# Kernel optimization log

Measured on AMD Instinct MI355X. Metric: run time of the kernel, lower is better.

The kernel has to match this reference:

```python
import jax, jax.numpy as jnp
import numpy as np

NEG_INF = -9e15  # matches torch's -9000000000000000.0 mask value
ALPHA = 0.2      # LeakyReLU negative slope


def setup_inputs() -> dict:
    key = jax.random.key(0)
    k1, k2, k3, k4 = jax.random.split(key, 4)
    B, N, Fin, Fout, H = 32, 512, 256, 64, 8
    x = jax.random.normal(k1, (B, N, Fin), dtype=jnp.float32)
    adj = (jax.random.uniform(k2, (B, N, N)) < 0.5).astype(jnp.float32)
    # W: Linear(in_features, out_features*n_heads, bias=False) weight, stored as (Fin, Fout*H)
    W = jax.random.normal(k3, (Fin, Fout * H), dtype=jnp.float32) / np.sqrt(Fin).astype(np.float32)
    # a: attention vector per head over concat(src,dst) features -> (H, 2*Fout)
    a = jax.random.normal(k4, (H, 2 * Fout), dtype=jnp.float32) * 0.1
    return {"x": x, "adj": adj, "W": W, "a": a}


def reference(x, adj, W, a):
    # x: (B,N,Fin), adj: (B,N,N), W: (Fin, H*F), a: (H, 2F)
    B, N, _ = x.shape
    H, twoF = a.shape
    F = twoF // 2
    h = (x @ W).reshape(B, N, H, F)  # (B,N,H,F)
    # Decompose concat-score: e_ij = lrelu(h_i . a_src + h_j . a_dst) -- same math
    # as (cat(h_i,h_j) * a).sum(-1) without materializing (B,N,N,H,2F).
    s_src = jnp.einsum('bnhf,hf->bnh', h, a[:, :F])  # (B,N,H)
    s_dst = jnp.einsum('bnhf,hf->bnh', h, a[:, F:])  # (B,N,H)
    e = s_src[:, :, None, :] + s_dst[:, None, :, :]  # (B,N,N,H)
    e = jax.nn.leaky_relu(e, negative_slope=ALPHA)
    e = jnp.where(adj[..., None] > 0, e, NEG_INF)
    attn = jax.nn.softmax(e, axis=2)  # softmax over neighbors j (dim=2)
    # dropout omitted (eval mode / p effectively 0 for the reference baseline)
    h_prime = jnp.einsum('bijh,bjhf->bihf', attn, h)  # (B,N,H,F)
    return h_prime.reshape(B, N, H * F)  # concat=True
```

## Files before the change

kernel.cpp:

```cpp
#include <hip/hip_runtime.h>
#include <hip/hip_bf16.h>


#define ALPHA  0.2f
#define ESCALE 1.4426950408889634f

typedef __bf16 bf16x8 __attribute__((ext_vector_type(8)));
typedef __bf16 bf16x4 __attribute__((ext_vector_type(4)));
typedef float  f32x4  __attribute__((ext_vector_type(4)));

#if __has_builtin(__builtin_amdgcn_exp2f)
#define EXP2(x) __builtin_amdgcn_exp2f(x)
#else
#define EXP2(x) exp2f(x)
#endif

#define HT_STRIDE 520
#define WT_STRIDE 264

struct Smem {
    __bf16 hT[64][HT_STRIDE];
    __bf16 WT[64][WT_STRIDE];
    float  ssrc[512], sdst[512];
    float  asrc[64], adst[64];
};

__device__ inline bf16x8 ld8(const float* p) {
    float4 a0 = *(const float4*)p;
    float4 a1 = *(const float4*)(p + 4);
    bf16x8 r;
    r[0]=(__bf16)a0.x; r[1]=(__bf16)a0.y; r[2]=(__bf16)a0.z; r[3]=(__bf16)a0.w;
    r[4]=(__bf16)a1.x; r[5]=(__bf16)a1.y; r[6]=(__bf16)a1.z; r[7]=(__bf16)a1.w;
    return r;
}

__global__ __launch_bounds__(1024, 4) void k_gat(const float* __restrict__ x,
                                                 const float* __restrict__ adj,
                                                 const float* __restrict__ W,
                                                 const float* __restrict__ a,
                                                 float* __restrict__ out) {
    __shared__ Smem sm;
    const int b = blockIdx.x, h = blockIdx.y;
    const int tid  = threadIdx.x;
    const int wave = tid >> 6, lane = tid & 63;
    const int quad = lane >> 4, col = lane & 15;

    if (tid < 128) {
        float v = a[h * 128 + tid] * ESCALE;
        if (tid < 64) sm.asrc[tid] = v; else sm.adst[tid - 64] = v;
    }
    {
        int c = tid & 63, k0 = tid >> 6;
        #pragma unroll 4
        for (int t = 0; t < 16; ++t)
            sm.WT[c][k0 + t * 16] = (__bf16)W[(long)(k0 + t * 16) * 512 + h * 64 + c];
    }
    __syncthreads();

    {
        const float* xb = x + (long)b * 512 * 256;
        f32x4 acc[2][4] = {};
        for (int ks = 0; ks < 8; ++ks) {
            int k0 = ks * 32 + quad * 8;
            bf16x8 av[2], bv[4];
            #pragma unroll
            for (int it = 0; it < 2; ++it)
                av[it] = ld8(xb + (long)(wave * 32 + it * 16 + col) * 256 + k0);
            #pragma unroll
            for (int nt = 0; nt < 4; ++nt)
                bv[nt] = *(const bf16x8*)(&sm.WT[nt * 16 + col][k0]);
            #pragma unroll
            for (int it = 0; it < 2; ++it)
                #pragma unroll
                for (int nt = 0; nt < 4; ++nt)
                    acc[it][nt] = __builtin_amdgcn_mfma_f32_16x16x32_bf16(av[it], bv[nt], acc[it][nt], 0, 0, 0);
        }
        #pragma unroll
        for (int it = 0; it < 2; ++it)
            #pragma unroll
            for (int nt = 0; nt < 4; ++nt) {
                int f = nt * 16 + col;
                int j = wave * 32 + it * 16 + quad * 4;
                bf16x4 pk = { (__bf16)acc[it][nt][0], (__bf16)acc[it][nt][1],
                              (__bf16)acc[it][nt][2], (__bf16)acc[it][nt][3] };
                *(bf16x4*)(&sm.hT[f][j]) = pk;
            }
    }
    __syncthreads();

    {
        int j = tid & 511;
        float s = 0.f;
        if (tid < 512) {
            #pragma unroll 8
            for (int f = 0; f < 64; ++f)
                s += (float)sm.hT[f][j] * sm.asrc[f];
            sm.ssrc[j] = s;
        } else {
            #pragma unroll 8
            for (int f = 0; f < 64; ++f)
                s += (float)sm.hT[f][j] * sm.adst[f];
            sm.sdst[j] = s;
        }
    }
    __syncthreads();

    {
        float si[2];
        const float* arow[2];
        #pragma unroll
        for (int it = 0; it < 2; ++it) {
            int i = wave * 32 + it * 16 + col;
            si[it]   = sm.ssrc[i];
            arow[it] = adj + ((long)b * 512 + i) * 512;
        }
        bf16x8 ones;
        #pragma unroll
        for (int u = 0; u < 8; ++u) ones[u] = (__bf16)1.0f;

        f32x4 acc[2][4] = {};
        f32x4 accs[2]   = {};
        float4 pa0[2], pa1[2];
        #pragma unroll
        for (int it = 0; it < 2; ++it) {
            pa0[it] = *(const float4*)(arow[it] + quad * 8);
            pa1[it] = *(const float4*)(arow[it] + quad * 8 + 4);
        }
        for (int ks = 0; ks < 16; ++ks) {
            int j0 = ks * 32 + quad * 8;
            f32x4 s0 = *(const f32x4*)&sm.sdst[j0];
            f32x4 s1 = *(const f32x4*)&sm.sdst[j0 + 4];
            float sd[8] = {s0[0],s0[1],s0[2],s0[3],s1[0],s1[1],s1[2],s1[3]};
            float am[2][8];
            #pragma unroll
            for (int it = 0; it < 2; ++it) {
                am[it][0]=pa0[it].x; am[it][1]=pa0[it].y;
                am[it][2]=pa0[it].z; am[it][3]=pa0[it].w;
                am[it][4]=pa1[it].x; am[it][5]=pa1[it].y;
                am[it][6]=pa1[it].z; am[it][7]=pa1[it].w;
            }
            if (ks < 15) {
                #pragma unroll
                for (int it = 0; it < 2; ++it) {
                    pa0[it] = *(const float4*)(arow[it] + j0 + 32);
                    pa1[it] = *(const float4*)(arow[it] + j0 + 36);
                }
            }
            bf16x8 P[2];
            #pragma unroll
            for (int it = 0; it < 2; ++it)
                #pragma unroll
                for (int u = 0; u < 8; ++u) {
                    float e = si[it] + sd[u];
                    float l = fmaxf(e, ALPHA * e);
                    float p = am[it][u] * EXP2(l);
                    P[it][u] = (__bf16)p;
                }
            bf16x8 bv[4];
            #pragma unroll
            for (int nt = 0; nt < 4; ++nt)
                bv[nt] = *(const bf16x8*)(&sm.hT[nt * 16 + col][j0]);
            #pragma unroll
            for (int it = 0; it < 2; ++it) {
                #pragma unroll
                for (int nt = 0; nt < 4; ++nt)
                    acc[it][nt] = __builtin_amdgcn_mfma_f32_16x16x32_bf16(P[it], bv[nt], acc[it][nt], 0, 0, 0);
                accs[it] = __builtin_amdgcn_mfma_f32_16x16x32_bf16(P[it], ones, accs[it], 0, 0, 0);
            }
        }
        #pragma unroll
        for (int it = 0; it < 2; ++it)
            #pragma unroll
            for (int r = 0; r < 4; ++r) {
                float s = accs[it][r];
                float inv = (s > 0.f) ? 1.0f / s : 0.f;
                int i = wave * 32 + it * 16 + quad * 4 + r;
                float* orow = out + ((long)b * 512 + i) * 512 + h * 64;
                #pragma unroll
                for (int nt = 0; nt < 4; ++nt)
                    orow[nt * 16 + col] = acc[it][nt][r] * inv;
            }
    }
}

extern "C" void kernel_launch(void* const* d_in, const int* in_sizes, int n_in,
                              void* d_out, int out_size, void* d_ws, size_t ws_size,
                              hipStream_t stream) {
    const float* x   = (const float*)d_in[0];
    const float* adj = (const float*)d_in[1];
    const float* W   = (const float*)d_in[2];
    const float* a   = (const float*)d_in[3];
    float* out = (float*)d_out;
    (void)d_ws; (void)ws_size;

    k_gat<<<dim3(32, 8), 1024, 0, stream>>>(x, adj, W, a, out);
}
```

Measured before the change: 141.2 us.

## Split each (batch, head) block into two 512-thread halves over query rows

Launches twice as many blocks of 512 threads, each handling half of the 512 query rows for a (batch, head) pair. Each block still recomputes the full projected features h and the attention scores, and the hT and WT shared buffers are now a union to cut LDS use. The intent is better occupancy and CU coverage (512 blocks instead of 256). The cost is that the x@W projection is computed twice per pair, and an extra barrier is needed before reusing the union storage.

```diff
diff --git a/kernel.cpp b/kernel.cpp
--- a/kernel.cpp
+++ b/kernel.cpp
@@ -19,8 +19,10 @@
 #define WT_STRIDE 264
 
 struct Smem {
-    __bf16 hT[64][HT_STRIDE];
-    __bf16 WT[64][WT_STRIDE];
+    union {
+        __bf16 hT[64][HT_STRIDE];
+        __bf16 WT[64][WT_STRIDE];
+    } u;
     float  ssrc[512], sdst[512];
     float  asrc[64], adst[64];
 };
@@ -34,13 +36,15 @@
     return r;
 }
 
-__global__ __launch_bounds__(1024, 4) void k_gat(const float* __restrict__ x,
-                                                 const float* __restrict__ adj,
-                                                 const float* __restrict__ W,
-                                                 const float* __restrict__ a,
-                                                 float* __restrict__ out) {
+__global__ __launch_bounds__(512, 4) void k_gat(const float* __restrict__ x,
+                                                const float* __restrict__ adj,
+                                                const float* __restrict__ W,
+                                                const float* __restrict__ a,
+                                                float* __restrict__ out) {
     __shared__ Smem sm;
-    const int b = blockIdx.x, h = blockIdx.y;
+    const int b    = blockIdx.x;
+    const int h    = blockIdx.y >> 1;
+    const int half = blockIdx.y & 1;
     const int tid  = threadIdx.x;
     const int wave = tid >> 6, lane = tid & 63;
     const int quad = lane >> 4, col = lane & 15;
@@ -52,65 +56,65 @@
     {
         int c = tid & 63, k0 = tid >> 6;
         #pragma unroll 4
-        for (int t = 0; t < 16; ++t)
-            sm.WT[c][k0 + t * 16] = (__bf16)W[(long)(k0 + t * 16) * 512 + h * 64 + c];
-    }
-    __syncthreads();
-
+        for (int t = 0; t < 32; ++t)
+            sm.u.WT[c][k0 + t * 8] = (__bf16)W[(long)(k0 + t * 8) * 512 + h * 64 + c];
+    }
+    __syncthreads();
+
+    f32x4 acc1[4][4] = {};
     {
         const float* xb = x + (long)b * 512 * 256;
-        f32x4 acc[2][4] = {};
         for (int ks = 0; ks < 8; ++ks) {
             int k0 = ks * 32 + quad * 8;
-            bf16x8 av[2], bv[4];
-            #pragma unroll
-            for (int it = 0; it < 2; ++it)
-                av[it] = ld8(xb + (long)(wave * 32 + it * 16 + col) * 256 + k0);
+            bf16x8 av[4], bv[4];
+            #pragma unroll
+            for (int it = 0; it < 4; ++it)
+                av[it] = ld8(xb + (long)(wave * 64 + it * 16 + col) * 256 + k0);
             #pragma unroll
             for (int nt = 0; nt < 4; ++nt)
-                bv[nt] = *(const bf16x8*)(&sm.WT[nt * 16 + col][k0]);
-            #pragma unroll
-            for (int it = 0; it < 2; ++it)
+                bv[nt] = *(const bf16x8*)(&sm.u.WT[nt * 16 + col][k0]);
+            #pragma unroll
+            for (int it = 0; it < 4; ++it)
                 #pragma unroll
                 for (int nt = 0; nt < 4; ++nt)
-                    acc[it][nt] = __builtin_amdgcn_mfma_f32_16x16x32_bf16(av[it], bv[nt], acc[it][nt], 0, 0, 0);
-        }
-        #pragma unroll
-        for (int it = 0; it < 2; ++it)
+                    acc1[it][nt] = __builtin_amdgcn_mfma_f32_16x16x32_bf16(av[it], bv[nt], acc1[it][nt], 0, 0, 0);
+        }
+    }
+    __syncthreads();
+    {
+        #pragma unroll
+        for (int it = 0; it < 4; ++it)
             #pragma unroll
             for (int nt = 0; nt < 4; ++nt) {
                 int f = nt * 16 + col;
-                int j = wave * 32 + it * 16 + quad * 4;
-                bf16x4 pk = { (__bf16)acc[it][nt][0], (__bf16)acc[it][nt][1],
-                              (__bf16)acc[it][nt][2], (__bf16)acc[it][nt][3] };
-                *(bf16x4*)(&sm.hT[f][j]) = pk;
-            }
-    }
-    __syncthreads();
-
-    {
-        int j = tid & 511;
-        float s = 0.f;
-        if (tid < 512) {
-            #pragma unroll 8
-            for (int f = 0; f < 64; ++f)
-                s += (float)sm.hT[f][j] * sm.asrc[f];
-            sm.ssrc[j] = s;
-        } else {
-            #pragma unroll 8
-            for (int f = 0; f < 64; ++f)
-                s += (float)sm.hT[f][j] * sm.adst[f];
-            sm.sdst[j] = s;
-        }
-    }
-    __syncthreads();
-
-    {
+                int j = wave * 64 + it * 16 + quad * 4;
+                bf16x4 pk = { (__bf16)acc1[it][nt][0], (__bf16)acc1[it][nt][1],
+                              (__bf16)acc1[it][nt][2], (__bf16)acc1[it][nt][3] };
+                *(bf16x4*)(&sm.u.hT[f][j]) = pk;
+            }
+    }
+    __syncthreads();
+
+    {
+        float as = 0.f, ad = 0.f;
+        #pragma unroll 8
+        for (int f = 0; f < 64; ++f) {
+            float v = (float)sm.u.hT[f][tid];
+            as += v * sm.asrc[f];
+            ad += v * sm.adst[f];
+        }
+        sm.ssrc[tid] = as;
+        sm.sdst[tid] = ad;
+    }
+    __syncthreads();
+
+    {
+        const int row0 = half * 256 + wave * 32;
         float si[2];
         const float* arow[2];
         #pragma unroll
         for (int it = 0; it < 2; ++it) {
-            int i = wave * 32 + it * 16 + col;
+            int i = row0 + it * 16 + col;
             si[it]   = sm.ssrc[i];
             arow[it] = adj + ((long)b * 512 + i) * 512;
         }
@@ -159,7 +163,7 @@
             bf16x8 bv[4];
             #pragma unroll
             for (int nt = 0; nt < 4; ++nt)
-                bv[nt] = *(const bf16x8*)(&sm.hT[nt * 16 + col][j0]);
+                bv[nt] = *(const bf16x8*)(&sm.u.hT[nt * 16 + col][j0]);
             #pragma unroll
             for (int it = 0; it < 2; ++it) {
                 #pragma unroll
@@ -174,7 +178,7 @@
             for (int r = 0; r < 4; ++r) {
                 float s = accs[it][r];
                 float inv = (s > 0.f) ? 1.0f / s : 0.f;
-                int i = wave * 32 + it * 16 + quad * 4 + r;
+                int i = row0 + it * 16 + quad * 4 + r;
                 float* orow = out + ((long)b * 512 + i) * 512 + h * 64;
                 #pragma unroll
                 for (int nt = 0; nt < 4; ++nt)
@@ -193,5 +197,5 @@
     float* out = (float*)d_out;
     (void)d_ws; (void)ws_size;
 
-    k_gat<<<dim3(32, 8), 1024, 0, stream>>>(x, adj, W, a, out);
+    k_gat<<<dim3(32, 16), 512, 0, stream>>>(x, adj, W, a, out);
 }
```

After: 153.6 us. 8.8% more time.

## Split GAT kernel into projection GEMM and row-tiled attention kernels via workspace

Applied to the files above, without the earlier changes.

Splits the fused kernel into two. The first computes the projected features h (bf16, transposed) plus per-node src/dst scores into workspace, computing the scores with shuffles instead of a shared-memory pass. The second launches 4x more, smaller blocks (row quarters) for the masked softmax and aggregation, reading h from global/L2 instead of LDS. This is meant to raise occupancy and parallelism beyond 256 large blocks, at the cost of a global round trip for h and a second launch. The old fused kernel is kept as a fallback when the workspace is too small.

```diff
diff --git a/kernel.cpp b/kernel.cpp
--- a/kernel.cpp
+++ b/kernel.cpp
@@ -17,13 +17,6 @@
 
 #define HT_STRIDE 520
 #define WT_STRIDE 264
-
-struct Smem {
-    __bf16 hT[64][HT_STRIDE];
-    __bf16 WT[64][WT_STRIDE];
-    float  ssrc[512], sdst[512];
-    float  asrc[64], adst[64];
-};
 
 __device__ inline bf16x8 ld8(const float* p) {
     float4 a0 = *(const float4*)p;
@@ -34,12 +27,18 @@
     return r;
 }
 
-__global__ __launch_bounds__(1024, 4) void k_gat(const float* __restrict__ x,
-                                                 const float* __restrict__ adj,
-                                                 const float* __restrict__ W,
-                                                 const float* __restrict__ a,
-                                                 float* __restrict__ out) {
-    __shared__ Smem sm;
+struct SmemK1 {
+    __bf16 WT[64][WT_STRIDE];
+    float  asrc[64], adst[64];
+};
+
+__global__ __launch_bounds__(512, 4) void k1_gemm(const float* __restrict__ x,
+                                                  const float* __restrict__ W,
+                                                  const float* __restrict__ a,
+                                                  __bf16* __restrict__ hT,
+                                                  float* __restrict__ ssrc,
+                                                  float* __restrict__ sdst) {
+    __shared__ SmemK1 sm;
     const int b = blockIdx.x, h = blockIdx.y;
     const int tid  = threadIdx.x;
     const int wave = tid >> 6, lane = tid & 63;
@@ -52,11 +51,200 @@
     {
         int c = tid & 63, k0 = tid >> 6;
         #pragma unroll 4
+        for (int t = 0; t < 32; ++t)
+            sm.WT[c][k0 + t * 8] = (__bf16)W[(long)(k0 + t * 8) * 512 + h * 64 + c];
+    }
+    __syncthreads();
+
+    f32x4 acc[4][4] = {};
+    {
+        const float* xb = x + (long)b * 512 * 256;
+        for (int ks = 0; ks < 8; ++ks) {
+            int k0 = ks * 32 + quad * 8;
+            bf16x8 av[4], bv[4];
+            #pragma unroll
+            for (int it = 0; it < 4; ++it)
+                av[it] = ld8(xb + (long)(wave * 64 + it * 16 + col) * 256 + k0);
+            #pragma unroll
+            for (int nt = 0; nt < 4; ++nt)
+                bv[nt] = *(const bf16x8*)(&sm.WT[nt * 16 + col][k0]);
+            #pragma unroll
+            for (int it = 0; it < 4; ++it)
+                #pragma unroll
+                for (int nt = 0; nt < 4; ++nt)
+                    acc[it][nt] = __builtin_amdgcn_mfma_f32_16x16x32_bf16(av[it], bv[nt], acc[it][nt], 0, 0, 0);
+        }
+    }
+
+    const long bh = (long)b * 8 + h;
+    {
+        #pragma unroll
+        for (int it = 0; it < 4; ++it)
+            #pragma unroll
+            for (int nt = 0; nt < 4; ++nt) {
+                int f = nt * 16 + col;
+                int j = wave * 64 + it * 16 + quad * 4;
+                bf16x4 pk = { (__bf16)acc[it][nt][0], (__bf16)acc[it][nt][1],
+                              (__bf16)acc[it][nt][2], (__bf16)acc[it][nt][3] };
+                *(bf16x4*)(hT + (bh * 64 + f) * 512 + j) = pk;
+            }
+    }
+
+    {
+        float asr[4], adr[4];
+        #pragma unroll
+        for (int nt = 0; nt < 4; ++nt) {
+            asr[nt] = sm.asrc[nt * 16 + col];
+            adr[nt] = sm.adst[nt * 16 + col];
+        }
+        #pragma unroll
+        for (int it = 0; it < 4; ++it)
+            #pragma unroll
+            for (int r = 0; r < 4; ++r) {
+                float ps = 0.f, pd = 0.f;
+                #pragma unroll
+                for (int nt = 0; nt < 4; ++nt) {
+                    ps += acc[it][nt][r] * asr[nt];
+                    pd += acc[it][nt][r] * adr[nt];
+                }
+                #pragma unroll
+                for (int m = 1; m <= 8; m <<= 1) {
+                    ps += __shfl_xor(ps, m, 64);
+                    pd += __shfl_xor(pd, m, 64);
+                }
+                if (col == 0) {
+                    int j = wave * 64 + it * 16 + quad * 4 + r;
+                    ssrc[bh * 512 + j] = ps;
+                    sdst[bh * 512 + j] = pd;
+                }
+            }
+    }
+}
+
+__global__ __launch_bounds__(256, 4) void k2_attn(const float* __restrict__ adj,
+                                                  const __bf16* __restrict__ hT,
+                                                  const float* __restrict__ ssrc,
+                                                  const float* __restrict__ sdst,
+                                                  float* __restrict__ out) {
+    __shared__ float sds[512];
+    const int b = blockIdx.x, h = blockIdx.y, q = blockIdx.z;
+    const int tid  = threadIdx.x;
+    const int wave = tid >> 6, lane = tid & 63;
+    const int quad = lane >> 4, col = lane & 15;
+    const long bh = (long)b * 8 + h;
+    const int rowbase = q * 128 + wave * 32;
+
+    sds[tid]       = sdst[bh * 512 + tid];
+    sds[tid + 256] = sdst[bh * 512 + tid + 256];
+
+    float si[2];
+    const float* arow[2];
+    #pragma unroll
+    for (int it = 0; it < 2; ++it) {
+        int i = rowbase + it * 16 + col;
+        si[it]   = ssrc[bh * 512 + i];
+        arow[it] = adj + ((long)b * 512 + i) * 512;
+    }
+    __syncthreads();
+
+    bf16x8 ones;
+    #pragma unroll
+    for (int u = 0; u < 8; ++u) ones[u] = (__bf16)1.0f;
+
+    f32x4 acc[2][4] = {};
+    f32x4 accs[2]   = {};
+    float4 pa0[2], pa1[2];
+    #pragma unroll
+    for (int it = 0; it < 2; ++it) {
+        pa0[it] = *(const float4*)(arow[it] + quad * 8);
+        pa1[it] = *(const float4*)(arow[it] + quad * 8 + 4);
+    }
+    const __bf16* hTb = hT + bh * 64 * 512;
+    for (int ks = 0; ks < 16; ++ks) {
+        int j0 = ks * 32 + quad * 8;
+        f32x4 s0 = *(const f32x4*)&sds[j0];
+        f32x4 s1 = *(const f32x4*)&sds[j0 + 4];
+        float sd[8] = {s0[0],s0[1],s0[2],s0[3],s1[0],s1[1],s1[2],s1[3]};
+        float am[2][8];
+        #pragma unroll
+        for (int it = 0; it < 2; ++it) {
+            am[it][0]=pa0[it].x; am[it][1]=pa0[it].y;
+            am[it][2]=pa0[it].z; am[it][3]=pa0[it].w;
+            am[it][4]=pa1[it].x; am[it][5]=pa1[it].y;
+            am[it][6]=pa1[it].z; am[it][7]=pa1[it].w;
+        }
+        if (ks < 15) {
+            #pragma unroll
+            for (int it = 0; it < 2; ++it) {
+                pa0[it] = *(const float4*)(arow[it] + j0 + 32);
+                pa1[it] = *(const float4*)(arow[it] + j0 + 36);
+            }
+        }
+        bf16x8 P[2];
+        #pragma unroll
+        for (int it = 0; it < 2; ++it)
+            #pragma unroll
+            for (int u = 0; u < 8; ++u) {
+                float e = si[it] + sd[u];
+                float l = fmaxf(e, ALPHA * e);
+                float p = am[it][u] * EXP2(l);
+                P[it][u] = (__bf16)p;
+            }
+        bf16x8 bv[4];
+        #pragma unroll
+        for (int nt = 0; nt < 4; ++nt)
+            bv[nt] = *(const bf16x8*)(hTb + (long)(nt * 16 + col) * 512 + j0);
+        #pragma unroll
+        for (int it = 0; it < 2; ++it) {
+            #pragma unroll
+            for (int nt = 0; nt < 4; ++nt)
+                acc[it][nt] = __builtin_amdgcn_mfma_f32_16x16x32_bf16(P[it], bv[nt], acc[it][nt], 0, 0, 0);
+            accs[it] = __builtin_amdgcn_mfma_f32_16x16x32_bf16(P[it], ones, accs[it], 0, 0, 0);
+        }
+    }
+    #pragma unroll
+    for (int it = 0; it < 2; ++it)
+        #pragma unroll
+        for (int r = 0; r < 4; ++r) {
+            float s = accs[it][r];
+            float inv = (s > 0.f) ? 1.0f / s : 0.f;
+            int i = rowbase + it * 16 + quad * 4 + r;
+            float* orow = out + ((long)b * 512 + i) * 512 + h * 64;
+            #pragma unroll
+            for (int nt = 0; nt < 4; ++nt)
+                orow[nt * 16 + col] = acc[it][nt][r] * inv;
+        }
+}
+
+struct SmemF {
+    __bf16 hT[64][HT_STRIDE];
+    __bf16 WT[64][WT_STRIDE];
+    float  ssrc[512], sdst[512];
+    float  asrc[64], adst[64];
+};
+
+__global__ __launch_bounds__(1024, 4) void k_gat_fused(const float* __restrict__ x,
+                                                       const float* __restrict__ adj,
+                                                       const float* __restrict__ W,
+                                                       const float* __restrict__ a,
+                                                       float* __restrict__ out) {
+    __shared__ SmemF sm;
+    const int b = blockIdx.x, h = blockIdx.y;
+    const int tid  = threadIdx.x;
+    const int wave = tid >> 6, lane = tid & 63;
+    const int quad = lane >> 4, col = lane & 15;
+
+    if (tid < 128) {
+        float v = a[h * 128 + tid] * ESCALE;
+        if (tid < 64) sm.asrc[tid] = v; else sm.adst[tid - 64] = v;
+    }
+    {
+        int c = tid & 63, k0 = tid >> 6;
+        #pragma unroll 4
         for (int t = 0; t < 16; ++t)
             sm.WT[c][k0 + t * 16] = (__bf16)W[(long)(k0 + t * 16) * 512 + h * 64 + c];
     }
     __syncthreads();
-
     {
         const float* xb = x + (long)b * 512 * 256;
         f32x4 acc[2][4] = {};
@@ -87,24 +275,20 @@
             }
     }
     __syncthreads();
-
     {
         int j = tid & 511;
         float s = 0.f;
         if (tid < 512) {
             #pragma unroll 8
-            for (int f = 0; f < 64; ++f)
-                s += (float)sm.hT[f][j] * sm.asrc[f];
+            for (int f = 0; f < 64; ++f) s += (float)sm.hT[f][j] * sm.asrc[f];
             sm.ssrc[j] = s;
         } else {
             #pragma unroll 8
-            for (int f = 0; f < 64; ++f)
-                s += (float)sm.hT[f][j] * sm.adst[f];
+            for (int f = 0; f < 64; ++f) s += (float)sm.hT[f][j] * sm.adst[f];
             sm.sdst[j] = s;
         }
     }
     __syncthreads();
-
     {
         float si[2];
         const float* arow[2];
@@ -117,7 +301,6 @@
         bf16x8 ones;
         #pragma unroll
         for (int u = 0; u < 8; ++u) ones[u] = (__bf16)1.0f;
-
         f32x4 acc[2][4] = {};
         f32x4 accs[2]   = {};
         float4 pa0[2], pa1[2];
@@ -191,7 +374,18 @@
     const float* W   = (const float*)d_in[2];
     const float* a   = (const float*)d_in[3];
     float* out = (float*)d_out;
-    (void)d_ws; (void)ws_size;
-
-    k_gat<<<dim3(32, 8), 1024, 0, stream>>>(x, adj, W, a, out);
-}
+
+    const size_t HT_BYTES = 32ull * 8 * 64 * 512 * 2;
+    const size_t SC_BYTES = 32ull * 8 * 512 * 4;
+    const size_t NEED = HT_BYTES + 2 * SC_BYTES;
+
+    if (d_ws && ws_size >= NEED) {
+        __bf16* hT  = (__bf16*)d_ws;
+        float* ssrc = (float*)((char*)d_ws + HT_BYTES);
+        float* sdst = ssrc + 32 * 8 * 512;
+        k1_gemm<<<dim3(32, 8), 512, 0, stream>>>(x, W, a, hT, ssrc, sdst);
+        k2_attn<<<dim3(32, 8, 4), 256, 0, stream>>>(adj, hT, ssrc, sdst, out);
+    } else {
+        k_gat_fused<<<dim3(32, 8), 1024, 0, stream>>>(x, adj, W, a, out);
+    }
+}
```

Measured after the change: 178.1 us. 26.2% more time.
